# Performance work log

Measured on AMD Instinct MI355X. Metric: run time of the kernel, lower is better.

The kernel has to match this reference:

```python
import jax, jax.numpy as jnp
import numpy as np

# dims: L=seq_len, N=batch, C=embed_dim, H=heads, D=head_dim, W=window_size
L, N, C, H, D, W = 1024, 4, 2048, 16, 128, 512
ROPE_BASE = 10000.0
SCALE = 1.0 / np.sqrt(D).astype(np.float32)


def _rope(x, cos, sin):
    # interleaved-pair rotary embedding; x: (..., D), cos/sin broadcast to (..., D//2)
    x1, x2 = x[..., 0::2], x[..., 1::2]
    return jnp.stack([x1 * cos - x2 * sin, x1 * sin + x2 * cos], axis=-1).reshape(x.shape)


def setup_inputs() -> dict:
    key = jax.random.key(0)
    ks = jax.random.split(key, 4)
    s = 0.02
    return {
        "x": jax.random.normal(ks[0], (L, N, C), jnp.float32),
        "wq": jax.random.normal(ks[1], (C, C), jnp.float32) * s,
        "bq": jnp.zeros((C,), jnp.float32),
        "wkv": jax.random.normal(ks[2], (2 * C, C), jnp.float32) * s,
        "bkv": jnp.zeros((2 * C,), jnp.float32),
        "wo": jax.random.normal(ks[3], (C, C), jnp.float32) * s,
        "bo": jnp.zeros((C,), jnp.float32),
        "alibi_slopes": jnp.asarray(2.0 ** (-8.0 * np.arange(1, H + 1) / H), jnp.float32),
    }


def reference(x, wq, bq, wkv, bkv, wo, bo, alibi_slopes):
    # x: (L, N, C) -> batch-major (N, L, C)
    xb = jnp.transpose(x, (1, 0, 2))
    q = (xb @ wq.T + bq).reshape(N, L, H, D)
    # memory=None path: zero input cache, cache_mask all False
    cache = jnp.zeros((N, W, C), x.dtype)
    kv_cache = cache @ wkv.T + bkv          # detached in original; masked out anyway
    kv_cur = xb @ wkv.T + bkv
    kv = jnp.concatenate([kv_cache, kv_cur], axis=1).reshape(N, L + W, 2, H, D)
    # RoPE over absolute kv positions [0, L+W); queries live at positions [W, W+L)
    t = jnp.arange(L + W, dtype=jnp.float32)
    inv_freq = 1.0 / (ROPE_BASE ** (jnp.arange(0, D, 2, dtype=jnp.float32) / D))
    freqs = jnp.outer(t, inv_freq)          # (L+W, D//2)
    cos, sin = jnp.cos(freqs), jnp.sin(freqs)
    q = _rope(q, cos[W:W + L][None, :, None, :], sin[W:W + L][None, :, None, :])
    k = _rope(kv[:, :, 0], cos[None, :, None, :], sin[None, :, None, :])
    v = kv[:, :, 1]
    scores = jnp.einsum('bihd,bjhd->bhij', q, k) * SCALE  # (N,H,L,L+W)
    i = jnp.arange(L)[:, None]
    j = jnp.arange(L + W)[None, :]
    # causal sliding window: query at kv-position i+W attends j in [i, i+W];
    # kv_mask is False for the (empty) cache region j < W
    mask = (j >= i) & (j <= i + W) & (j >= W)
    bias = alibi_slopes[:, None, None] * (j - i - W).astype(jnp.float32)  # <= 0 in window
    scores = jnp.where(mask[None, None], scores + bias[None], -jnp.inf)
    p = jax.nn.softmax(scores, axis=-1)
    attn = jnp.einsum('bhij,bjhd->bihd', p, v).reshape(N, L, C)
    out = attn @ wo.T + bo
    return jnp.transpose(out, (1, 0, 2))    # (L, N, C)
```

## Files before the change

### kernel.cpp

```cpp
#include <hip/hip_runtime.h>
#include <hip/hip_bf16.h>

typedef __attribute__((ext_vector_type(4))) float f32x4;
typedef __attribute__((ext_vector_type(8))) short s16x8;
typedef __attribute__((ext_vector_type(4))) short s16x4;
typedef __attribute__((ext_vector_type(4))) int i32x4;

__device__ __forceinline__ short f2bf(float f) {
    union { __hip_bfloat16 h; short s; } u;
    u.h = __float2bfloat16(f);
    return u.s;
}

#define GLD16(g, l) __builtin_amdgcn_global_load_lds((const __attribute__((address_space(1))) void*)(g), (__attribute__((address_space(3))) void*)(l), 16, 0, 0)
#define MFMA16(a, b, c) __builtin_amdgcn_mfma_f32_16x16x32_bf16((a), (b), (c), 0, 0, 0)

__global__ void conv_lin(const float* __restrict__ in, short* __restrict__ out, int n4) {
    int i = blockIdx.x * blockDim.x + threadIdx.x;
    int stride = gridDim.x * blockDim.x;
    for (; i < n4; i += stride) {
        float4 v = reinterpret_cast<const float4*>(in)[i];
        s16x4 o;
        o[0] = f2bf(v.x); o[1] = f2bf(v.y); o[2] = f2bf(v.z); o[3] = f2bf(v.w);
        reinterpret_cast<s16x4*>(out)[i] = o;
    }
}

__global__ void conv_x(const float* __restrict__ x, short* __restrict__ Xb) {
    const int total = 1024 * 4 * 2048 / 4;
    int i = blockIdx.x * blockDim.x + threadIdx.x;
    int stride = gridDim.x * blockDim.x;
    for (; i < total; i += stride) {
        float4 v = reinterpret_cast<const float4*>(x)[i];
        int c4 = i & 511;
        int n  = (i >> 9) & 3;
        int l  = i >> 11;
        s16x4 o;
        o[0] = f2bf(v.x); o[1] = f2bf(v.y); o[2] = f2bf(v.z); o[3] = f2bf(v.w);
        reinterpret_cast<s16x4*>(Xb)[(n * 1024 + l) * 512 + c4] = o;
    }
}

__global__ void rope_tab(float* __restrict__ ctab, float* __restrict__ stab) {
    int l = blockIdx.x, t = threadIdx.x;
    float pos = (float)(512 + l);
    float inv = __expf(-9.210340371976184f * ((float)t * (1.0f / 64.0f)));
    float a = pos * inv;
    float s, c;
    sincosf(a, &s, &c);
    ctab[l * 64 + t] = c;
    stab[l * 64 + t] = s;
}


__device__ __forceinline__ void stage_t(const short* __restrict__ G, int rowbase, int kt,
                                        short* dst, int tid, int q) {
    int chunk = q * 512 + tid;
    int row = chunk >> 3;
    int c = ((chunk & 7) << 4) ^ ((row & 7) << 4);
    GLD16(G + (size_t)(rowbase + row) * 2048 + kt + (c >> 1), dst + (q * 512 + (tid & ~63)) * 8);
}

__device__ __forceinline__ s16x8 rd_frag(const short* buf, int row, int ks, int lane) {
    int byte = row * 128 + (((ks << 6) + ((lane >> 4) << 4)) ^ ((row & 7) << 4));
    return *reinterpret_cast<const s16x8*>(reinterpret_cast<const char*>(buf) + byte);
}

__device__ __forceinline__ void gemm_core(const short* __restrict__ A, const short* __restrict__ B,
                                          short* Ab0, short* Ab1, short* Bb0, short* Bb1,
                                          f32x4 acc[4][4], int m0, int j0) {
    const int tid = threadIdx.x, lane = tid & 63;
    const int w = tid >> 6, wr = w >> 1, wc = w & 1;

    stage_t(A, m0, 0, Ab0, tid, 0); stage_t(A, m0, 0, Ab0, tid, 1);
    stage_t(A, m0, 0, Ab0, tid, 2); stage_t(A, m0, 0, Ab0, tid, 3);
    stage_t(B, j0, 0, Bb0, tid, 0); stage_t(B, j0, 0, Bb0, tid, 1);
    __syncthreads();

    for (int t = 0; t < 32; ++t) {
        const short* As = (t & 1) ? Ab1 : Ab0;
        const short* Bs = (t & 1) ? Bb1 : Bb0;
        short* An = (t & 1) ? Ab0 : Ab1;
        short* Bn = (t & 1) ? Bb0 : Bb1;
        const int ktn = (t + 1) << 6;
        const bool pf = (t < 31);

        s16x8 a0[4], b0[4];
        #pragma unroll
        for (int mi = 0; mi < 4; ++mi) a0[mi] = rd_frag(As, wr * 64 + mi * 16 + (lane & 15), 0, lane);
        #pragma unroll
        for (int nj = 0; nj < 4; ++nj) b0[nj] = rd_frag(Bs, wc * 64 + nj * 16 + (lane & 15), 0, lane);
        if (pf) { stage_t(A, m0, ktn, An, tid, 0); stage_t(A, m0, ktn, An, tid, 1); }
        __builtin_amdgcn_s_setprio(1);
        #pragma unroll
        for (int mi = 0; mi < 4; ++mi)
            #pragma unroll
            for (int nj = 0; nj < 4; ++nj)
                acc[mi][nj] = MFMA16(a0[mi], b0[nj], acc[mi][nj]);
        __builtin_amdgcn_s_setprio(0);
        if (pf) { stage_t(A, m0, ktn, An, tid, 2); stage_t(A, m0, ktn, An, tid, 3); }

        s16x8 a1[4], b1[4];
        #pragma unroll
        for (int mi = 0; mi < 4; ++mi) a1[mi] = rd_frag(As, wr * 64 + mi * 16 + (lane & 15), 1, lane);
        #pragma unroll
        for (int nj = 0; nj < 4; ++nj) b1[nj] = rd_frag(Bs, wc * 64 + nj * 16 + (lane & 15), 1, lane);
        if (pf) { stage_t(B, j0, ktn, Bn, tid, 0); stage_t(B, j0, ktn, Bn, tid, 1); }
        __builtin_amdgcn_s_setprio(1);
        #pragma unroll
        for (int mi = 0; mi < 4; ++mi)
            #pragma unroll
            for (int nj = 0; nj < 4; ++nj)
                acc[mi][nj] = MFMA16(a1[mi], b1[nj], acc[mi][nj]);
        __builtin_amdgcn_s_setprio(0);
        __syncthreads();
    }
}

__global__ __launch_bounds__(512, 2)
void gemm_qkv2(const short* __restrict__ Xb, const short* __restrict__ Wqkv,
               const float* __restrict__ bq, const float* __restrict__ bkv,
               const float* __restrict__ ctab, const float* __restrict__ stab,
               short* __restrict__ Qr, short* __restrict__ Kr, short* __restrict__ Vr) {
    __shared__ short Ab0[256 * 64], Ab1[256 * 64], Bb0[128 * 64], Bb1[128 * 64];
    int b = blockIdx.x;
    int work = (b & 7) * 96 + (b >> 3);
    const int m0 = (work & 15) * 256;
    const int j0 = (work >> 4) * 128;

    f32x4 acc[4][4];
    #pragma unroll
    for (int a = 0; a < 4; ++a)
        #pragma unroll
        for (int c = 0; c < 4; ++c)
            #pragma unroll
            for (int r = 0; r < 4; ++r) acc[a][c][r] = 0.f;
    gemm_core(Xb, Wqkv, Ab0, Ab1, Bb0, Bb1, acc, m0, j0);

    const int tid = threadIdx.x, lane = tid & 63, w = tid >> 6;
    const int wr = w >> 1, wc = w & 1;
    const int region = j0 >> 11;
    #pragma unroll
    for (int mi = 0; mi < 4; ++mi) {
        #pragma unroll
        for (int nj = 0; nj < 4; ++nj) {
            int col = j0 + wc * 64 + nj * 16 + (lane & 15);
            int h = (col >> 7) & 15;
            int d = col & 127;
            #pragma unroll
            for (int r = 0; r < 4; ++r) {
                int row = m0 + wr * 64 + mi * 16 + (lane >> 4) * 4 + r;
                int n = row >> 10, l = row & 1023;
                float v = acc[mi][nj][r];
                size_t oidx = (((size_t)(n * 16 + h)) * 1024 + l) * 128 + d;
                if (region == 0) {
                    v += bq[col];
                    float other = __shfl_xor(v, 1, 64);
                    float cs = ctab[l * 64 + (d >> 1)];
                    float sn = stab[l * 64 + (d >> 1)];
                    float o = (d & 1) ? (other * sn + v * cs) : (v * cs - other * sn);
                    Qr[oidx] = f2bf(o * 0.08838834764831843f);
                } else if (region == 1) {
                    v += bkv[col - 2048];
                    float other = __shfl_xor(v, 1, 64);
                    float cs = ctab[l * 64 + (d >> 1)];
                    float sn = stab[l * 64 + (d >> 1)];
                    float o = (d & 1) ? (other * sn + v * cs) : (v * cs - other * sn);
                    Kr[oidx] = f2bf(o);
                } else {
                    v += bkv[col - 2048];
                    Vr[oidx] = f2bf(v);
                }
            }
        }
    }
}

__global__ __launch_bounds__(512, 2)
void gemm_out2(const short* __restrict__ Attn, const short* __restrict__ Wo,
               const float* __restrict__ bo, float* __restrict__ out) {
    __shared__ short Ab0[256 * 64], Ab1[256 * 64], Bb0[128 * 64], Bb1[128 * 64];
    int b = blockIdx.x;
    int work = (b & 7) * 32 + (b >> 3);
    const int m0 = (work & 15) * 256;
    const int j0 = (work >> 4) * 128;

    f32x4 acc[4][4];
    #pragma unroll
    for (int a = 0; a < 4; ++a)
        #pragma unroll
        for (int c = 0; c < 4; ++c)
            #pragma unroll
            for (int r = 0; r < 4; ++r) acc[a][c][r] = 0.f;
    gemm_core(Attn, Wo, Ab0, Ab1, Bb0, Bb1, acc, m0, j0);

    const int tid = threadIdx.x, lane = tid & 63, w = tid >> 6;
    const int wr = w >> 1, wc = w & 1;
    #pragma unroll
    for (int mi = 0; mi < 4; ++mi)
        #pragma unroll
        for (int nj = 0; nj < 4; ++nj) {
            int col = j0 + wc * 64 + nj * 16 + (lane & 15);
            #pragma unroll
            for (int r = 0; r < 4; ++r) {
                int row = m0 + wr * 64 + mi * 16 + (lane >> 4) * 4 + r;
                int n = row >> 10, l = row & 1023;
                out[((size_t)(l * 4 + n)) * 2048 + col] = acc[mi][nj][r] + bo[col];
            }
        }
}

__global__ __launch_bounds__(256, 1)
void attn_fwd(const short* __restrict__ Qr, const short* __restrict__ Kr,
              const short* __restrict__ Vr, const float* __restrict__ slopes,
              short* __restrict__ Attn) {
    __shared__ short Ks[64 * 128];
    __shared__ short Vts[128 * 64];
    __shared__ short Ps[4][2048];

    const int i0 = blockIdx.x * 128;
    const int nh = blockIdx.y;
    const int n = nh >> 4, h = nh & 15;
    const short* Qh = Qr + (size_t)nh * (1024 * 128);
    const short* Kh = Kr + (size_t)nh * (1024 * 128);
    const short* Vh = Vr + (size_t)nh * (1024 * 128);
    const float slope = slopes[h];
    const int tid = threadIdx.x, lane = tid & 63, w = tid >> 6;

    s16x8 qf[2][4];
    #pragma unroll
    for (int mi = 0; mi < 2; ++mi)
        #pragma unroll
        for (int kk = 0; kk < 4; ++kk) {
            int row = i0 + w * 32 + mi * 16 + (lane & 15);
            qf[mi][kk] = *reinterpret_cast<const s16x8*>(Qh + (size_t)row * 128 + kk * 32 + (lane >> 4) * 8);
        }

    f32x4 oacc[2][8];
    #pragma unroll
    for (int mi = 0; mi < 2; ++mi)
        #pragma unroll
        for (int dj = 0; dj < 8; ++dj)
            #pragma unroll
            for (int r = 0; r < 4; ++r) oacc[mi][dj][r] = 0.f;
    float mrun[2][4], lrun[2][4];
    #pragma unroll
    for (int mi = 0; mi < 2; ++mi)
        #pragma unroll
        for (int r = 0; r < 4; ++r) { mrun[mi][r] = -1e30f; lrun[mi][r] = 0.f; }

    const int jlo = (i0 >= 512) ? (i0 - 512) : 0;
    const int jhi = i0 + 127;
    for (int j0 = jlo; j0 <= jhi; j0 += 64) {
        #pragma unroll
        for (int q = 0; q < 4; ++q) {
            int rbase = w * 16 + q * 4;
            int rloc = rbase + (lane >> 4);
            int lc = ((lane & 15) ^ (rloc & 7)) << 3;
            GLD16(Kh + (size_t)(j0 + rloc) * 128 + lc, Ks + rbase * 128);
        }
        #pragma unroll
        for (int p = 0; p < 4; ++p) {
            int d0 = (w + p * 4) * 8;
            int jj = j0 + lane;
            i32x4 vv = *reinterpret_cast<const i32x4*>(Vh + (size_t)jj * 128 + d0);
            const short* vs = reinterpret_cast<const short*>(&vv);
            #pragma unroll
            for (int e = 0; e < 8; ++e) {
                int d = d0 + e;
                int byte = d * 128 + ((lane * 2) ^ ((d & 7) << 4));
                *reinterpret_cast<short*>(reinterpret_cast<char*>(Vts) + byte) = vs[e];
            }
        }
        __syncthreads();

        f32x4 sacc[2][4];
        #pragma unroll
        for (int mi = 0; mi < 2; ++mi)
            #pragma unroll
            for (int nj = 0; nj < 4; ++nj)
                #pragma unroll
                for (int r = 0; r < 4; ++r) sacc[mi][nj][r] = 0.f;
        #pragma unroll
        for (int kk = 0; kk < 4; ++kk) {
            s16x8 kf[4];
            #pragma unroll
            for (int nj = 0; nj < 4; ++nj) {
                int kr = nj * 16 + (lane & 15);
                int byte = kr * 256 + ((kk * 64 + (lane >> 4) * 16) ^ ((kr & 7) << 4));
                kf[nj] = *reinterpret_cast<const s16x8*>(reinterpret_cast<const char*>(Ks) + byte);
            }
            #pragma unroll
            for (int mi = 0; mi < 2; ++mi)
                #pragma unroll
                for (int nj = 0; nj < 4; ++nj)
                    sacc[mi][nj] = MFMA16(qf[mi][kk], kf[nj], sacc[mi][nj]);
        }

        #pragma unroll
        for (int mi = 0; mi < 2; ++mi) {
            #pragma unroll
            for (int r = 0; r < 4; ++r) {
                int iq = i0 + w * 32 + mi * 16 + (lane >> 4) * 4 + r;
                float mx = -1e30f;
                #pragma unroll
                for (int nj = 0; nj < 4; ++nj) {
                    int jj = j0 + nj * 16 + (lane & 15);
                    float v = -1e30f;
                    if (jj <= iq && jj >= iq - 512)
                        v = sacc[mi][nj][r] + slope * (float)(jj - iq);
                    sacc[mi][nj][r] = v;
                    mx = fmaxf(mx, v);
                }
                #pragma unroll
                for (int s = 1; s < 16; s <<= 1) mx = fmaxf(mx, __shfl_xor(mx, s, 64));
                float mnew = fmaxf(mrun[mi][r], mx);
                float sf = __expf(mrun[mi][r] - mnew);
                mrun[mi][r] = mnew;
                lrun[mi][r] *= sf;
                #pragma unroll
                for (int dj = 0; dj < 8; ++dj) oacc[mi][dj][r] *= sf;
                float rs = 0.f;
                #pragma unroll
                for (int nj = 0; nj < 4; ++nj) {
                    float v = sacc[mi][nj][r];
                    float p = (v < -1e29f) ? 0.f : __expf(v - mnew);
                    sacc[mi][nj][r] = p;
                    rs += p;
                }
                #pragma unroll
                for (int s = 1; s < 16; s <<= 1) rs += __shfl_xor(rs, s, 64);
                lrun[mi][r] += rs;
            }
        }

        char* Pw = reinterpret_cast<char*>(&Ps[w][0]);
        #pragma unroll
        for (int mi = 0; mi < 2; ++mi)
            #pragma unroll
            for (int nj = 0; nj < 4; ++nj)
                #pragma unroll
                for (int r = 0; r < 4; ++r) {
                    int prow = mi * 16 + (lane >> 4) * 4 + r;
                    int cb = (nj * 16 + (lane & 15)) * 2;
                    int byte = prow * 128 + (cb ^ ((prow & 7) << 4));
                    *reinterpret_cast<short*>(Pw + byte) = f2bf(sacc[mi][nj][r]);
                }

        #pragma unroll
        for (int ks = 0; ks < 2; ++ks) {
            s16x8 pf[2];
            #pragma unroll
            for (int mi = 0; mi < 2; ++mi) {
                int prow = mi * 16 + (lane & 15);
                int byte = prow * 128 + (((ks * 32 + (lane >> 4) * 8) * 2) ^ ((prow & 7) << 4));
                pf[mi] = *reinterpret_cast<const s16x8*>(Pw + byte);
            }
            #pragma unroll
            for (int dj = 0; dj < 8; ++dj) {
                int d = dj * 16 + (lane & 15);
                int byte = d * 128 + (((ks * 32 + (lane >> 4) * 8) * 2) ^ ((d & 7) << 4));
                s16x8 vf = *reinterpret_cast<const s16x8*>(reinterpret_cast<const char*>(Vts) + byte);
                #pragma unroll
                for (int mi = 0; mi < 2; ++mi)
                    oacc[mi][dj] = MFMA16(pf[mi], vf, oacc[mi][dj]);
            }
        }
        __syncthreads();
    }

    #pragma unroll
    for (int mi = 0; mi < 2; ++mi)
        #pragma unroll
        for (int dj = 0; dj < 8; ++dj)
            #pragma unroll
            for (int r = 0; r < 4; ++r) {
                int iq = i0 + w * 32 + mi * 16 + (lane >> 4) * 4 + r;
                int d = dj * 16 + (lane & 15);
                float v = oacc[mi][dj][r] / lrun[mi][r];
                Attn[((size_t)(n * 1024 + iq)) * 2048 + h * 128 + d] = f2bf(v);
            }
}

extern "C" void kernel_launch(void* const* d_in, const int* in_sizes, int n_in,
                              void* d_out, int out_size, void* d_ws, size_t ws_size,
                              hipStream_t stream) {
    const float* x      = (const float*)d_in[0];
    const float* wq     = (const float*)d_in[1];
    const float* bq     = (const float*)d_in[2];
    const float* wkv    = (const float*)d_in[3];
    const float* bkv    = (const float*)d_in[4];
    const float* wo     = (const float*)d_in[5];
    const float* bo     = (const float*)d_in[6];
    const float* slopes = (const float*)d_in[7];
    float* out = (float*)d_out;

    char* ws = (char*)d_ws;
    size_t off = 0;
    auto alloc = [&](size_t bytes) { char* p = ws + off; off += (bytes + 255) & ~(size_t)255; return p; };
    float* ctab = (float*)alloc((size_t)1024 * 64 * 4);
    float* stab = (float*)alloc((size_t)1024 * 64 * 4);
    short* Xb   = (short*)alloc((size_t)4096 * 2048 * 2);
    short* Wqkv = (short*)alloc((size_t)6144 * 2048 * 2);
    short* Wo   = (short*)alloc((size_t)2048 * 2048 * 2);
    short* Qr   = (short*)alloc((size_t)64 * 1024 * 128 * 2);
    short* Kr   = (short*)alloc((size_t)64 * 1024 * 128 * 2);
    short* Vr   = (short*)alloc((size_t)64 * 1024 * 128 * 2);
    short* Attn = (short*)alloc((size_t)4096 * 2048 * 2);

    conv_x<<<2048, 256, 0, stream>>>(x, Xb);
    conv_lin<<<1024, 256, 0, stream>>>(wq, Wqkv, 2048 * 2048 / 4);
    conv_lin<<<2048, 256, 0, stream>>>(wkv, Wqkv + (size_t)2048 * 2048, 4096 * 2048 / 4);
    conv_lin<<<1024, 256, 0, stream>>>(wo, Wo, 2048 * 2048 / 4);
    rope_tab<<<1024, 64, 0, stream>>>(ctab, stab);
    gemm_qkv2<<<768, 512, 0, stream>>>(Xb, Wqkv, bq, bkv, ctab, stab, Qr, Kr, Vr);
    attn_fwd<<<dim3(8, 64), 256, 0, stream>>>(Qr, Kr, Vr, slopes, Attn);
    gemm_out2<<<256, 512, 0, stream>>>(Attn, Wo, bo, out);
}
```

Measured before the change: 288.6 us.

## Triple-buffer GEMM LDS pipeline with explicit waitcnt and remap block-to-tile order

Replaces the double-buffered GEMM main loop with a three-stage LDS ring that prefetches two K-tiles ahead. Explicit vmcnt/lgkmcnt waits and sched barriers control when loads land, and each iteration splits into two half-M MFMA phases with the next tile's loads interleaved. The block-to-tile mapping is also changed so each group of 8 blocks shares an M row band while spanning different N columns. The goal is to hide global-load latency and improve L2 reuse, at the cost of 50% more LDS (144KB per block) and extra barriers, which may limit occupancy to one block per CU.

Result: slower. 366.3 us (+26.9%).

```diff
diff --git a/kernel.cpp b/kernel.cpp
--- a/kernel.cpp
+++ b/kernel.cpp
@@ -66,67 +66,115 @@
     return *reinterpret_cast<const s16x8*>(reinterpret_cast<const char*>(buf) + byte);
 }
 
-__device__ __forceinline__ void gemm_core(const short* __restrict__ A, const short* __restrict__ B,
-                                          short* Ab0, short* Ab1, short* Bb0, short* Bb1,
-                                          f32x4 acc[4][4], int m0, int j0) {
+#define BARS() do { __builtin_amdgcn_s_barrier(); __builtin_amdgcn_sched_barrier(0); } while (0)
+
+__device__ __forceinline__ void gemm_core3(const short* __restrict__ A, const short* __restrict__ B,
+                                           short* AL, short* BL, f32x4 acc[4][4], int m0, int j0) {
     const int tid = threadIdx.x, lane = tid & 63;
     const int w = tid >> 6, wr = w >> 1, wc = w & 1;
 
-    stage_t(A, m0, 0, Ab0, tid, 0); stage_t(A, m0, 0, Ab0, tid, 1);
-    stage_t(A, m0, 0, Ab0, tid, 2); stage_t(A, m0, 0, Ab0, tid, 3);
-    stage_t(B, j0, 0, Bb0, tid, 0); stage_t(B, j0, 0, Bb0, tid, 1);
-    __syncthreads();
-
-    for (int t = 0; t < 32; ++t) {
-        const short* As = (t & 1) ? Ab1 : Ab0;
-        const short* Bs = (t & 1) ? Bb1 : Bb0;
-        short* An = (t & 1) ? Ab0 : Ab1;
-        short* Bn = (t & 1) ? Bb0 : Bb1;
-        const int ktn = (t + 1) << 6;
-        const bool pf = (t < 31);
-
-        s16x8 a0[4], b0[4];
-        #pragma unroll
-        for (int mi = 0; mi < 4; ++mi) a0[mi] = rd_frag(As, wr * 64 + mi * 16 + (lane & 15), 0, lane);
-        #pragma unroll
-        for (int nj = 0; nj < 4; ++nj) b0[nj] = rd_frag(Bs, wc * 64 + nj * 16 + (lane & 15), 0, lane);
-        if (pf) { stage_t(A, m0, ktn, An, tid, 0); stage_t(A, m0, ktn, An, tid, 1); }
+    #pragma unroll
+    for (int q = 0; q < 4; ++q) stage_t(A, m0, 0, AL, tid, q);
+    stage_t(B, j0, 0, BL, tid, 0); stage_t(B, j0, 0, BL, tid, 1);
+    #pragma unroll
+    for (int q = 0; q < 4; ++q) stage_t(A, m0, 64, AL + 16384, tid, q);
+    stage_t(B, j0, 64, BL + 8192, tid, 0); stage_t(B, j0, 64, BL + 8192, tid, 1);
+
+    for (int t = 0; t < 31; ++t) {
+        const int s = t % 3, sn = (t + 2) % 3;
+        const short* Asl = AL + s * 16384;
+        const short* Bsl = BL + s * 8192;
+        short* Asn = AL + sn * 16384;
+        short* Bsn = BL + sn * 8192;
+        const int ktn = (t + 2) << 6;
+        const bool st = (t <= 29);
+
+        if (st) { stage_t(A, m0, ktn, Asn, tid, 0); stage_t(A, m0, ktn, Asn, tid, 1);
+                  stage_t(B, j0, ktn, Bsn, tid, 0); }
+        asm volatile("s_waitcnt vmcnt(9)" ::: "memory");
+        BARS();
+        s16x8 bfr[4][2], afr[2][2];
+        #pragma unroll
+        for (int nj = 0; nj < 4; ++nj) {
+            bfr[nj][0] = rd_frag(Bsl, wc * 64 + nj * 16 + (lane & 15), 0, lane);
+            bfr[nj][1] = rd_frag(Bsl, wc * 64 + nj * 16 + (lane & 15), 1, lane);
+        }
+        #pragma unroll
+        for (int mi = 0; mi < 2; ++mi) {
+            afr[mi][0] = rd_frag(Asl, wr * 64 + mi * 16 + (lane & 15), 0, lane);
+            afr[mi][1] = rd_frag(Asl, wr * 64 + mi * 16 + (lane & 15), 1, lane);
+        }
+        asm volatile("s_waitcnt lgkmcnt(0)" ::: "memory");
+        __builtin_amdgcn_sched_barrier(0);
         __builtin_amdgcn_s_setprio(1);
         #pragma unroll
-        for (int mi = 0; mi < 4; ++mi)
-            #pragma unroll
-            for (int nj = 0; nj < 4; ++nj)
-                acc[mi][nj] = MFMA16(a0[mi], b0[nj], acc[mi][nj]);
+        for (int ks = 0; ks < 2; ++ks)
+            #pragma unroll
+            for (int mi = 0; mi < 2; ++mi)
+                #pragma unroll
+                for (int nj = 0; nj < 4; ++nj)
+                    acc[mi][nj] = MFMA16(afr[mi][ks], bfr[nj][ks], acc[mi][nj]);
         __builtin_amdgcn_s_setprio(0);
-        if (pf) { stage_t(A, m0, ktn, An, tid, 2); stage_t(A, m0, ktn, An, tid, 3); }
-
-        s16x8 a1[4], b1[4];
-        #pragma unroll
-        for (int mi = 0; mi < 4; ++mi) a1[mi] = rd_frag(As, wr * 64 + mi * 16 + (lane & 15), 1, lane);
-        #pragma unroll
-        for (int nj = 0; nj < 4; ++nj) b1[nj] = rd_frag(Bs, wc * 64 + nj * 16 + (lane & 15), 1, lane);
-        if (pf) { stage_t(B, j0, ktn, Bn, tid, 0); stage_t(B, j0, ktn, Bn, tid, 1); }
+        BARS();
+
+        if (st) { stage_t(A, m0, ktn, Asn, tid, 2); stage_t(A, m0, ktn, Asn, tid, 3);
+                  stage_t(B, j0, ktn, Bsn, tid, 1); }
+        s16x8 afr2[2][2];
+        #pragma unroll
+        for (int mi = 0; mi < 2; ++mi) {
+            afr2[mi][0] = rd_frag(Asl, wr * 64 + (mi + 2) * 16 + (lane & 15), 0, lane);
+            afr2[mi][1] = rd_frag(Asl, wr * 64 + (mi + 2) * 16 + (lane & 15), 1, lane);
+        }
+        asm volatile("s_waitcnt lgkmcnt(0)" ::: "memory");
+        __builtin_amdgcn_sched_barrier(0);
         __builtin_amdgcn_s_setprio(1);
         #pragma unroll
-        for (int mi = 0; mi < 4; ++mi)
-            #pragma unroll
-            for (int nj = 0; nj < 4; ++nj)
-                acc[mi][nj] = MFMA16(a1[mi], b1[nj], acc[mi][nj]);
+        for (int ks = 0; ks < 2; ++ks)
+            #pragma unroll
+            for (int mi = 0; mi < 2; ++mi)
+                #pragma unroll
+                for (int nj = 0; nj < 4; ++nj)
+                    acc[mi + 2][nj] = MFMA16(afr2[mi][ks], bfr[nj][ks], acc[mi + 2][nj]);
         __builtin_amdgcn_s_setprio(0);
-        __syncthreads();
+        BARS();
+    }
+
+    {
+        const short* Asl = AL + (31 % 3) * 16384;
+        const short* Bsl = BL + (31 % 3) * 8192;
+        asm volatile("s_waitcnt vmcnt(0)" ::: "memory");
+        BARS();
+        s16x8 bfr[4][2];
+        #pragma unroll
+        for (int nj = 0; nj < 4; ++nj) {
+            bfr[nj][0] = rd_frag(Bsl, wc * 64 + nj * 16 + (lane & 15), 0, lane);
+            bfr[nj][1] = rd_frag(Bsl, wc * 64 + nj * 16 + (lane & 15), 1, lane);
+        }
+        #pragma unroll
+        for (int mi = 0; mi < 4; ++mi) {
+            s16x8 a0 = rd_frag(Asl, wr * 64 + mi * 16 + (lane & 15), 0, lane);
+            s16x8 a1 = rd_frag(Asl, wr * 64 + mi * 16 + (lane & 15), 1, lane);
+            asm volatile("s_waitcnt lgkmcnt(0)" ::: "memory");
+            __builtin_amdgcn_sched_barrier(0);
+            #pragma unroll
+            for (int nj = 0; nj < 4; ++nj) acc[mi][nj] = MFMA16(a0, bfr[nj][0], acc[mi][nj]);
+            #pragma unroll
+            for (int nj = 0; nj < 4; ++nj) acc[mi][nj] = MFMA16(a1, bfr[nj][1], acc[mi][nj]);
+        }
     }
 }
 
 __global__ __launch_bounds__(512, 2)
-void gemm_qkv2(const short* __restrict__ Xb, const short* __restrict__ Wqkv,
+void gemm_qkv3(const short* __restrict__ Xb, const short* __restrict__ Wqkv,
                const float* __restrict__ bq, const float* __restrict__ bkv,
                const float* __restrict__ ctab, const float* __restrict__ stab,
                short* __restrict__ Qr, short* __restrict__ Kr, short* __restrict__ Vr) {
-    __shared__ short Ab0[256 * 64], Ab1[256 * 64], Bb0[128 * 64], Bb1[128 * 64];
+    __shared__ short AL[3 * 16384];
+    __shared__ short BL[3 * 8192];
     int b = blockIdx.x;
-    int work = (b & 7) * 96 + (b >> 3);
-    const int m0 = (work & 15) * 256;
-    const int j0 = (work >> 4) * 128;
+    int i = b >> 3;
+    const int m0 = (i / 6) * 256;
+    const int j0 = ((i % 6) + (b & 7) * 6) * 128;
 
     f32x4 acc[4][4];
     #pragma unroll
@@ -135,7 +183,7 @@
         for (int c = 0; c < 4; ++c)
             #pragma unroll
             for (int r = 0; r < 4; ++r) acc[a][c][r] = 0.f;
-    gemm_core(Xb, Wqkv, Ab0, Ab1, Bb0, Bb1, acc, m0, j0);
+    gemm_core3(Xb, Wqkv, AL, BL, acc, m0, j0);
 
     const int tid = threadIdx.x, lane = tid & 63, w = tid >> 6;
     const int wr = w >> 1, wc = w & 1;
@@ -177,13 +225,14 @@
 }
 
 __global__ __launch_bounds__(512, 2)
-void gemm_out2(const short* __restrict__ Attn, const short* __restrict__ Wo,
+void gemm_out3(const short* __restrict__ Attn, const short* __restrict__ Wo,
                const float* __restrict__ bo, float* __restrict__ out) {
-    __shared__ short Ab0[256 * 64], Ab1[256 * 64], Bb0[128 * 64], Bb1[128 * 64];
+    __shared__ short AL[3 * 16384];
+    __shared__ short BL[3 * 8192];
     int b = blockIdx.x;
-    int work = (b & 7) * 32 + (b >> 3);
-    const int m0 = (work & 15) * 256;
-    const int j0 = (work >> 4) * 128;
+    int i = b >> 3;
+    const int m0 = (i / 2) * 256;
+    const int j0 = ((i % 2) + (b & 7) * 2) * 128;
 
     f32x4 acc[4][4];
     #pragma unroll
@@ -192,7 +241,7 @@
         for (int c = 0; c < 4; ++c)
             #pragma unroll
             for (int r = 0; r < 4; ++r) acc[a][c][r] = 0.f;
-    gemm_core(Attn, Wo, Ab0, Ab1, Bb0, Bb1, acc, m0, j0);
+    gemm_core3(Attn, Wo, AL, BL, acc, m0, j0);
 
     const int tid = threadIdx.x, lane = tid & 63, w = tid >> 6;
     const int wr = w >> 1, wc = w & 1;
@@ -413,7 +462,7 @@
     conv_lin<<<2048, 256, 0, stream>>>(wkv, Wqkv + (size_t)2048 * 2048, 4096 * 2048 / 4);
     conv_lin<<<1024, 256, 0, stream>>>(wo, Wo, 2048 * 2048 / 4);
     rope_tab<<<1024, 64, 0, stream>>>(ctab, stab);
-    gemm_qkv2<<<768, 512, 0, stream>>>(Xb, Wqkv, bq, bkv, ctab, stab, Qr, Kr, Vr);
+    gemm_qkv3<<<768, 512, 0, stream>>>(Xb, Wqkv, bq, bkv, ctab, stab, Qr, Kr, Vr);
     attn_fwd<<<dim3(8, 64), 256, 0, stream>>>(Qr, Kr, Vr, slopes, Attn);
-    gemm_out2<<<256, 512, 0, stream>>>(Attn, Wo, bo, out);
-}
+    gemm_out3<<<256, 512, 0, stream>>>(Attn, Wo, bo, out);
+}
```
